# Performance work log

Measured on AMD Instinct MI355X. Metric: run time of the kernel, lower is better.

The kernel has to match this reference:

```python
import jax, jax.numpy as jnp
import numpy as np

N_SUPPORT = 4096
N_QUERY = 8192
H = W = 28
IN_DIM = H * W  # 784
EMBED_DIM = 512
N_CLASSES = 64


def setup_inputs() -> dict:
    key = jax.random.key(0)
    k1, k2, k3, k4 = jax.random.split(key, 4)
    support_set = jax.random.normal(k1, (N_SUPPORT, 1, H, W), dtype=jnp.float32)
    query_set = jax.random.normal(k2, (N_QUERY, 1, H, W), dtype=jnp.float32)
    # one-hot support labels (N, C)
    lbl = jax.random.randint(k3, (N_SUPPORT,), 0, N_CLASSES)
    support_labels = jax.nn.one_hot(lbl, N_CLASSES, dtype=jnp.float32)
    # encoder params: flatten + dense projection stand-in for embedding_net
    W_enc = jax.random.normal(k4, (IN_DIM, EMBED_DIM), dtype=jnp.float32) * (1.0 / np.sqrt(IN_DIM))
    b_enc = jnp.zeros((EMBED_DIM,), dtype=jnp.float32)
    return {
        "support_set": support_set,
        "query_set": query_set,
        "support_labels": support_labels,
        "W_enc": W_enc,
        "b_enc": b_enc,
    }


def _encode(x, W_enc, b_enc):
    # (B, 1, H, W) -> (B, D): flatten + linear projection
    B = x.shape[0]
    return x.reshape(B, -1) @ W_enc + b_enc


def _neg_cdist(q, s):
    # -euclidean distance, computed via the expansion ||q-s||^2 = |q|^2 + |s|^2 - 2 q.s
    q2 = jnp.sum(q * q, axis=-1, keepdims=True)          # (Q, 1)
    s2 = jnp.sum(s * s, axis=-1)[None, :]                # (1, N)
    qs = jnp.einsum("qd,nd->qn", q, s)                  # (Q, N)
    d2 = jnp.maximum(q2 + s2 - 2.0 * qs, 0.0)
    return -jnp.sqrt(d2)


def reference(support_set, query_set, support_labels, W_enc, b_enc):
    support_emb = _encode(support_set, W_enc, b_enc)     # (N, D)
    query_emb = _encode(query_set, W_enc, b_enc)         # (Q, D)
    distances = _neg_cdist(query_emb, support_emb)       # (Q, N)
    attention = jax.nn.softmax(distances, axis=1)        # (Q, N)
    predictions = attention @ support_labels             # (Q, C)
    return predictions
```

## Files before the change

### kernel.cpp

```cpp
#include <hip/hip_runtime.h>

#define N_SUP 4096
#define N_QRY 8192
#define IN_DIM 784
#define EMB 512
#define NCLS 64
#define M_TOT (N_SUP + N_QRY)
#define NCHUNK 25
#define XCH 13

typedef _Float16 f16;
typedef _Float16 f16x8 __attribute__((ext_vector_type(8)));
typedef float f32x4 __attribute__((ext_vector_type(4)));

#define GLDS16(gp, lp)                                                        \
    __builtin_amdgcn_global_load_lds(                                         \
        (const __attribute__((address_space(1))) void*)(gp),                  \
        (__attribute__((address_space(3))) void*)(lp), 16, 0, 0)

#define WAITB(N)                                                              \
    asm volatile("s_waitcnt vmcnt(" #N ")" ::: "memory");                     \
    __builtin_amdgcn_s_barrier();                                             \
    __builtin_amdgcn_sched_barrier(0);

static __device__ __forceinline__ f16x8 cvt8(const float* p) {
    float4 a = *(const float4*)p;
    float4 b = *(const float4*)(p + 4);
    f16x8 v;
    v[0] = (f16)a.x; v[1] = (f16)a.y; v[2] = (f16)a.z; v[3] = (f16)a.w;
    v[4] = (f16)b.x; v[5] = (f16)b.y; v[6] = (f16)b.z; v[7] = (f16)b.w;
    return v;
}

__global__ __launch_bounds__(256) void pre_enc(const float* __restrict__ W,
                                               const float* __restrict__ lab,
                                               f16* __restrict__ Wb,
                                               int* __restrict__ lbl) {
    if (blockIdx.x < 200) {
        int g = blockIdx.x * 256 + threadIdx.x;
        if (g >= NCHUNK * 32 * 64) return;
        int chunk = g >> 11;
        int rem = g & 2047;
        int nbg = rem >> 6, lane = rem & 63;
        int n = nbg * 16 + (lane & 15);
        int kbase = chunk * 32 + (lane >> 4) * 8;
        f16x8 v;
#pragma unroll
        for (int j = 0; j < 8; ++j) {
            int k = kbase + j;
            v[j] = (k < IN_DIM) ? (f16)W[(size_t)k * EMB + n] : (f16)0.f;
        }
        *(f16x8*)(Wb + (size_t)g * 8) = v;
    } else {
        const int w = threadIdx.x >> 6, lane = threadIdx.x & 63;
        const int s = (blockIdx.x - 200) * 4 + w;
        float v = lab[(size_t)s * NCLS + lane];
        int c = lane;
#pragma unroll
        for (int off = 1; off < 64; off <<= 1) {
            float v2 = __shfl_xor(v, off);
            int c2 = __shfl_xor(c, off);
            if (v2 > v || (v2 == v && c2 < c)) { v = v2; c = c2; }
        }
        if (lane == 0) lbl[s] = c;
    }
}

__global__ __launch_bounds__(256) void encode(
    const float* __restrict__ sup, const float* __restrict__ qry,
    const f16* __restrict__ Wb, const float* __restrict__ bias,
    f16* __restrict__ E, float* __restrict__ norms)
{
    __shared__ __align__(16) f16 Xs[32][72];
    const int tid = threadIdx.x;
    const int w = tid >> 6, lane = tid & 63;
    const int q = lane >> 4, c16 = lane & 15;
    const int mb = blockIdx.x >> 1;
    const int ch = blockIdx.x & 1;
    const int m0 = mb * 32;
    const int rbase = (w & 1) * 16;
    const int nbg0 = ch * 16 + (w >> 1) * 8;
    const int cbase = nbg0 * 16;

    f32x4 acc[8];
#pragma unroll
    for (int nb = 0; nb < 8; ++nb) acc[nb] = (f32x4){0.f, 0.f, 0.f, 0.f};

    const int sr = tid >> 3;
    const int sq = tid & 7;
    const float* xrow;
    {
        int gr = m0 + sr;
        xrow = (gr < N_SUP) ? sup + (size_t)gr * IN_DIM
                            : qry + (size_t)(gr - N_SUP) * IN_DIM;
    }

    f16x8 xg = cvt8(xrow + sq * 8);

    for (int c = 0; c < XCH; ++c) {
        __syncthreads();
        *(f16x8*)&Xs[sr][sq * 8] = xg;
        __syncthreads();
        if (c + 1 < XCH) {
            int k = (c + 1) * 64 + sq * 8;
            xg = (k + 8 <= IN_DIM) ? cvt8(xrow + k) : (f16x8){0,0,0,0,0,0,0,0};
        }
#pragma unroll
        for (int kc = 0; kc < 2; ++kc) {
            int c32 = c * 2 + kc;
            if (c32 >= NCHUNK) break;
            f16x8 a = *(const f16x8*)&Xs[rbase + c16][kc * 32 + q * 8];
            const f16* wb = Wb + ((size_t)(c32 * 32 + nbg0) * 64 + lane) * 8;
#pragma unroll
            for (int nb = 0; nb < 8; ++nb) {
                f16x8 b = *(const f16x8*)(wb + (size_t)nb * 512);
                acc[nb] = __builtin_amdgcn_mfma_f32_16x16x32_f16(a, b, acc[nb], 0, 0, 0);
            }
        }
    }

    float nrm[4] = {0.f, 0.f, 0.f, 0.f};
#pragma unroll
    for (int nb = 0; nb < 8; ++nb) {
        int col = cbase + nb * 16 + c16;
        float bv = bias[col];
#pragma unroll
        for (int r = 0; r < 4; ++r) {
            int row = m0 + rbase + q * 4 + r;
            float v = acc[nb][r] + bv;
            E[(size_t)row * EMB + col] = (f16)v;
            nrm[r] += v * v;
        }
    }
#pragma unroll
    for (int r = 0; r < 4; ++r) {
        float v = nrm[r];
        v += __shfl_xor(v, 1); v += __shfl_xor(v, 2);
        v += __shfl_xor(v, 4); v += __shfl_xor(v, 8);
        if (c16 == 0) atomicAdd(&norms[m0 + rbase + q * 4 + r], v);
    }
}

__global__ __launch_bounds__(256) void post_enc(
    const f16* __restrict__ E, const float* __restrict__ norms,
    const int* __restrict__ lbl, f16* __restrict__ Sb,
    f16* __restrict__ Lcs, float* __restrict__ manc)
{
    const int b = blockIdx.x;
    if (b < 1024) {
        int g = b * 256 + threadIdx.x;
        int s = g >> 6, lg = g & 63;
        f16x8 v = *(const f16x8*)(E + (size_t)s * EMB + lg * 8);
        *(f16x8*)(Sb + (size_t)s * EMB + ((lg ^ (s & 15)) * 8)) = v;
    } else if (b < 3072) {
        const int w = threadIdx.x >> 6, lane = threadIdx.x & 63;
        const int qrow = (b - 1024) * 4 + w;
        f16x8 qv = *(const f16x8*)(E + (size_t)(N_SUP + qrow) * EMB + lane * 8);
        f16x8 sv = *(const f16x8*)(E + lane * 8);
        float dot = 0.f;
#pragma unroll
        for (int j = 0; j < 8; ++j) dot += (float)qv[j] * (float)sv[j];
        dot += __shfl_xor(dot, 1);  dot += __shfl_xor(dot, 2);
        dot += __shfl_xor(dot, 4);  dot += __shfl_xor(dot, 8);
        dot += __shfl_xor(dot, 16); dot += __shfl_xor(dot, 32);
        if (lane == 0) {
            float d2 = fmaxf(norms[N_SUP + qrow] + norms[0] - 2.f * dot, 0.f);
            manc[qrow] = sqrtf(d2);
        }
    } else {
        int idx = (b - 3072) * 256 + threadIdx.x;
        int c = idx >> 12, s = idx & (N_SUP - 1);
        Lcs[idx] = (lbl[s] == c) ? (f16)1.f : (f16)0.f;
    }
}

__global__ __launch_bounds__(256, 2) void attn(
    const f16* __restrict__ E, const float* __restrict__ norms,
    const float* __restrict__ manc, const f16* __restrict__ Lcs,
    const f16* __restrict__ Sb, float* __restrict__ Num)
{
    __shared__ __align__(16) f16 Ss[4][16 * EMB];
    __shared__ __align__(16) f16 Pt[4][16][40];
    __shared__ float Sn[512];
    const int tid = threadIdx.x;
    const int w = tid >> 6, lane = tid & 63;
    const int q = lane >> 4, c16 = lane & 15;
    const int ss = blockIdx.x & 7;
    const int qt = blockIdx.x >> 3;

    Sn[tid]       = norms[ss * 512 + tid];
    Sn[256 + tid] = norms[ss * 512 + 256 + tid];

    f16x8 qf[16];
    const f16* qb = E + (size_t)(N_SUP + qt * 64 + w * 16 + c16) * EMB + q * 8;
#pragma unroll
    for (int ks = 0; ks < 16; ++ks) qf[ks] = *(const f16x8*)(qb + ks * 32);
    float q2[4], mrow[4];
#pragma unroll
    for (int r = 0; r < 4; ++r) {
        q2[r]   = norms[N_SUP + qt * 64 + w * 16 + q * 4 + r];
        mrow[r] = manc[qt * 64 + w * 16 + q * 4 + r];
    }

    f32x4 accPL[4];
#pragma unroll
    for (int nb = 0; nb < 4; ++nb) accPL[nb] = (f32x4){0.f, 0.f, 0.f, 0.f};

    const f16* sb_base = Sb + (size_t)(ss * 512) * EMB;
    const int wslot = w * 256;

    auto ISSUE = [&](int tt) {
        const f16* gsrc = sb_base + (size_t)tt * 16 * EMB;
#pragma unroll
        for (int i = 0; i < 4; ++i)
            GLDS16(gsrc + (size_t)(wslot + i * 64 + lane) * 8,
                   &Ss[tt & 3][(wslot + i * 64) * 8]);
    };
    auto BL = [&](int p, f16x8* bl) {
        const int ps0 = ss * 512 + p * 32;
#pragma unroll
        for (int nbc = 0; nbc < 4; ++nbc)
            bl[nbc] = *(const f16x8*)(Lcs + (size_t)(nbc * 16 + c16) * N_SUP + ps0 + q * 8);
    };
    auto QK = [&](int t) -> f32x4 {
        f32x4 a = (f32x4){0.f, 0.f, 0.f, 0.f};
        const f16* S = &Ss[t & 3][0];
#pragma unroll
        for (int kc = 0; kc < 4; ++kc)
#pragma unroll
            for (int ksl = 0; ksl < 4; ++ksl) {
                const int lg = kc * 16 + ksl * 4 + q;
                f16x8 b = *(const f16x8*)&S[c16 * EMB + ((lg ^ c16) * 8)];
                a = __builtin_amdgcn_mfma_f32_16x16x32_f16(qf[kc * 4 + ksl], b, a, 0, 0, 0);
            }
        return a;
    };
    auto EPI = [&](f32x4 acc, int t) {
        const float s2 = Sn[t * 16 + c16];
        const int pcol = (t & 1) * 16 + c16;
#pragma unroll
        for (int r = 0; r < 4; ++r) {
            float d2 = fmaxf(q2[r] + s2 - 2.f * acc[r], 0.f);
            float p = __expf(mrow[r] - __builtin_amdgcn_sqrtf(d2));
            Pt[w][q * 4 + r][pcol] = (f16)fminf(p, 60000.f);
        }
    };
    auto PV = [&](const f16x8* bl) {
        f16x8 af = *(const f16x8*)&Pt[w][c16][q * 8];
#pragma unroll
        for (int nbc = 0; nbc < 4; ++nbc)
            accPL[nbc] = __builtin_amdgcn_mfma_f32_16x16x32_f16(af, bl[nbc], accPL[nbc], 0, 0, 0);
    };

    ISSUE(0); ISSUE(1); ISSUE(2);
    asm volatile("s_waitcnt lgkmcnt(0)" ::: "memory");

    f16x8 bl[4];
    for (int tp = 0; tp < 14; ++tp) {
        const int t0 = tp * 2;
        WAITB(8);
        BL(tp, bl);
        ISSUE(t0 + 3);
        EPI(QK(t0), t0);
        WAITB(8);
        ISSUE(t0 + 4);
        EPI(QK(t0 + 1), t0 + 1);
        PV(bl);
    }
    WAITB(8); BL(14, bl); ISSUE(31); EPI(QK(28), 28);
    WAITB(8); EPI(QK(29), 29); PV(bl);
    WAITB(4); BL(15, bl); EPI(QK(30), 30);
    WAITB(0); EPI(QK(31), 31); PV(bl);

#pragma unroll
    for (int nbc = 0; nbc < 4; ++nbc)
#pragma unroll
        for (int r = 0; r < 4; ++r)
            atomicAdd(&Num[(size_t)(qt * 64 + w * 16 + q * 4 + r) * NCLS + nbc * 16 + c16],
                      accPL[nbc][r]);
}

__global__ __launch_bounds__(256) void finalize(const float* __restrict__ Num,
                                                float* __restrict__ out) {
    const int tid = threadIdx.x;
    const int w = tid >> 6, lane = tid & 63;
    const int qrow = blockIdx.x * 4 + w;
    float v = Num[(size_t)qrow * NCLS + lane];
    float s = v;
    s += __shfl_xor(s, 1);  s += __shfl_xor(s, 2);  s += __shfl_xor(s, 4);
    s += __shfl_xor(s, 8);  s += __shfl_xor(s, 16); s += __shfl_xor(s, 32);
    out[(size_t)qrow * NCLS + lane] = v / s;
}

extern "C" void kernel_launch(void* const* d_in, const int* in_sizes, int n_in,
                              void* d_out, int out_size, void* d_ws, size_t ws_size,
                              hipStream_t stream) {
    (void)in_sizes; (void)n_in; (void)out_size; (void)ws_size;
    const float* sup  = (const float*)d_in[0];
    const float* qry  = (const float*)d_in[1];
    const float* lab  = (const float*)d_in[2];
    const float* Wenc = (const float*)d_in[3];
    const float* benc = (const float*)d_in[4];
    float* out = (float*)d_out;

    char* ws = (char*)d_ws;
    size_t off = 0;
    f16* Wb = (f16*)(ws + off);        off += (size_t)NCHUNK * 32 * 64 * 8 * 2;
    f16* E  = (f16*)(ws + off);        off += (size_t)M_TOT * EMB * 2;
    f16* Sb = (f16*)(ws + off);        off += (size_t)N_SUP * EMB * 2;
    int* lbl = (int*)(ws + off);       off += (size_t)N_SUP * 4;
    f16* Lcs = (f16*)(ws + off);       off += (size_t)NCLS * N_SUP * 2;
    float* manc = (float*)(ws + off);  off += (size_t)N_QRY * 4;
    float* norms = (float*)(ws + off); off += (size_t)M_TOT * 4;
    float* Num = (float*)(ws + off);   off += (size_t)N_QRY * NCLS * 4;

    hipMemsetAsync(norms, 0, (size_t)M_TOT * 4 + (size_t)N_QRY * NCLS * 4, stream);

    pre_enc<<<1224, 256, 0, stream>>>(Wenc, lab, Wb, lbl);
    encode<<<M_TOT / 32 * 2, 256, 0, stream>>>(sup, qry, Wb, benc, E, norms);
    post_enc<<<4096, 256, 0, stream>>>(E, norms, lbl, Sb, Lcs, manc);
    attn<<<N_QRY / 64 * 8, 256, 0, stream>>>(E, norms, manc, Lcs, Sb, Num);
    finalize<<<N_QRY / 4, 256, 0, stream>>>(Num, out);
}
```

Baseline: 198.9 us.

## Fuse memset, anchor-distance and finalize into neighbouring kernels

Workspace zeroing (norms, Num, and a new per-tile counter) moves into extra blocks of pre_enc, replacing the hipMemsetAsync. The per-query anchor distance to support 0 is now computed inside attn from the already-loaded query fragments instead of in post_enc. The final row normalisation is done by the last of the eight attn blocks per query tile, using a threadfence and an atomic counter, which removes the finalize launch. Together these cut launches and intermediate global traffic, at the cost of extra redundant dot-product work per attn block and a serialized tail in the last block.

```diff
diff --git a/kernel.cpp b/kernel.cpp
--- a/kernel.cpp
+++ b/kernel.cpp
@@ -35,7 +35,8 @@
 __global__ __launch_bounds__(256) void pre_enc(const float* __restrict__ W,
                                                const float* __restrict__ lab,
                                                f16* __restrict__ Wb,
-                                               int* __restrict__ lbl) {
+                                               int* __restrict__ lbl,
+                                               float4* __restrict__ zbase) {
     if (blockIdx.x < 200) {
         int g = blockIdx.x * 256 + threadIdx.x;
         if (g >= NCHUNK * 32 * 64) return;
@@ -51,7 +52,7 @@
             v[j] = (k < IN_DIM) ? (f16)W[(size_t)k * EMB + n] : (f16)0.f;
         }
         *(f16x8*)(Wb + (size_t)g * 8) = v;
-    } else {
+    } else if (blockIdx.x < 1224) {
         const int w = threadIdx.x >> 6, lane = threadIdx.x & 63;
         const int s = (blockIdx.x - 200) * 4 + w;
         float v = lab[(size_t)s * NCLS + lane];
@@ -63,6 +64,9 @@
             if (v2 > v || (v2 == v && c2 < c)) { v = v2; c = c2; }
         }
         if (lane == 0) lbl[s] = c;
+    } else {
+        int idx = (blockIdx.x - 1224) * 256 + threadIdx.x;
+        zbase[idx] = (float4){0.f, 0.f, 0.f, 0.f};
     }
 }
 
@@ -142,9 +146,8 @@
 }
 
 __global__ __launch_bounds__(256) void post_enc(
-    const f16* __restrict__ E, const float* __restrict__ norms,
-    const int* __restrict__ lbl, f16* __restrict__ Sb,
-    f16* __restrict__ Lcs, float* __restrict__ manc)
+    const f16* __restrict__ E, const int* __restrict__ lbl,
+    f16* __restrict__ Sb, f16* __restrict__ Lcs)
 {
     const int b = blockIdx.x;
     if (b < 1024) {
@@ -152,23 +155,8 @@
         int s = g >> 6, lg = g & 63;
         f16x8 v = *(const f16x8*)(E + (size_t)s * EMB + lg * 8);
         *(f16x8*)(Sb + (size_t)s * EMB + ((lg ^ (s & 15)) * 8)) = v;
-    } else if (b < 3072) {
-        const int w = threadIdx.x >> 6, lane = threadIdx.x & 63;
-        const int qrow = (b - 1024) * 4 + w;
-        f16x8 qv = *(const f16x8*)(E + (size_t)(N_SUP + qrow) * EMB + lane * 8);
-        f16x8 sv = *(const f16x8*)(E + lane * 8);
-        float dot = 0.f;
-#pragma unroll
-        for (int j = 0; j < 8; ++j) dot += (float)qv[j] * (float)sv[j];
-        dot += __shfl_xor(dot, 1);  dot += __shfl_xor(dot, 2);
-        dot += __shfl_xor(dot, 4);  dot += __shfl_xor(dot, 8);
-        dot += __shfl_xor(dot, 16); dot += __shfl_xor(dot, 32);
-        if (lane == 0) {
-            float d2 = fmaxf(norms[N_SUP + qrow] + norms[0] - 2.f * dot, 0.f);
-            manc[qrow] = sqrtf(d2);
-        }
     } else {
-        int idx = (b - 3072) * 256 + threadIdx.x;
+        int idx = (b - 1024) * 256 + threadIdx.x;
         int c = idx >> 12, s = idx & (N_SUP - 1);
         Lcs[idx] = (lbl[s] == c) ? (f16)1.f : (f16)0.f;
     }
@@ -176,12 +164,14 @@
 
 __global__ __launch_bounds__(256, 2) void attn(
     const f16* __restrict__ E, const float* __restrict__ norms,
-    const float* __restrict__ manc, const f16* __restrict__ Lcs,
-    const f16* __restrict__ Sb, float* __restrict__ Num)
+    const f16* __restrict__ Lcs, const f16* __restrict__ Sb,
+    float* __restrict__ Num, int* __restrict__ cnt, float* __restrict__ out)
 {
     __shared__ __align__(16) f16 Ss[4][16 * EMB];
     __shared__ __align__(16) f16 Pt[4][16][40];
     __shared__ float Sn[512];
+    __shared__ float Manc[4][16];
+    __shared__ int lastf;
     const int tid = threadIdx.x;
     const int w = tid >> 6, lane = tid & 63;
     const int q = lane >> 4, c16 = lane & 15;
@@ -195,11 +185,27 @@
     const f16* qb = E + (size_t)(N_SUP + qt * 64 + w * 16 + c16) * EMB + q * 8;
 #pragma unroll
     for (int ks = 0; ks < 16; ++ks) qf[ks] = *(const f16x8*)(qb + ks * 32);
+
+    {
+        float n0 = norms[0];
+        float dp = 0.f;
+        const f16* s0p = E + q * 8;
+#pragma unroll
+        for (int ks = 0; ks < 16; ++ks) {
+            f16x8 sv = *(const f16x8*)(s0p + ks * 32);
+#pragma unroll
+            for (int j = 0; j < 8; ++j) dp += (float)qf[ks][j] * (float)sv[j];
+        }
+        dp += __shfl_xor(dp, 16);
+        dp += __shfl_xor(dp, 32);
+        float qn = norms[N_SUP + qt * 64 + w * 16 + c16];
+        Manc[w][c16] = __builtin_amdgcn_sqrtf(fmaxf(qn + n0 - 2.f * dp, 0.f));
+    }
     float q2[4], mrow[4];
 #pragma unroll
     for (int r = 0; r < 4; ++r) {
         q2[r]   = norms[N_SUP + qt * 64 + w * 16 + q * 4 + r];
-        mrow[r] = manc[qt * 64 + w * 16 + q * 4 + r];
+        mrow[r] = Manc[w][q * 4 + r];
     }
 
     f32x4 accPL[4];
@@ -278,18 +284,23 @@
         for (int r = 0; r < 4; ++r)
             atomicAdd(&Num[(size_t)(qt * 64 + w * 16 + q * 4 + r) * NCLS + nbc * 16 + c16],
                       accPL[nbc][r]);
-}
-
-__global__ __launch_bounds__(256) void finalize(const float* __restrict__ Num,
-                                                float* __restrict__ out) {
-    const int tid = threadIdx.x;
-    const int w = tid >> 6, lane = tid & 63;
-    const int qrow = blockIdx.x * 4 + w;
-    float v = Num[(size_t)qrow * NCLS + lane];
-    float s = v;
-    s += __shfl_xor(s, 1);  s += __shfl_xor(s, 2);  s += __shfl_xor(s, 4);
-    s += __shfl_xor(s, 8);  s += __shfl_xor(s, 16); s += __shfl_xor(s, 32);
-    out[(size_t)qrow * NCLS + lane] = v / s;
+
+    __threadfence();
+    if (tid == 0) lastf = (atomicAdd(cnt + qt, 1) == 7) ? 1 : 0;
+    __syncthreads();
+    if (lastf) {
+        const float* Nq = Num + (size_t)(qt * 64) * NCLS;
+        float* oq = out + (size_t)(qt * 64) * NCLS;
+#pragma unroll
+        for (int i = 0; i < 16; ++i) {
+            int row = w * 16 + i;
+            float v = Nq[row * NCLS + lane];
+            float s = v;
+            s += __shfl_xor(s, 1);  s += __shfl_xor(s, 2);  s += __shfl_xor(s, 4);
+            s += __shfl_xor(s, 8);  s += __shfl_xor(s, 16); s += __shfl_xor(s, 32);
+            oq[row * NCLS + lane] = v / s;
+        }
+    }
 }
 
 extern "C" void kernel_launch(void* const* d_in, const int* in_sizes, int n_in,
@@ -310,15 +321,12 @@
     f16* Sb = (f16*)(ws + off);        off += (size_t)N_SUP * EMB * 2;
     int* lbl = (int*)(ws + off);       off += (size_t)N_SUP * 4;
     f16* Lcs = (f16*)(ws + off);       off += (size_t)NCLS * N_SUP * 2;
-    float* manc = (float*)(ws + off);  off += (size_t)N_QRY * 4;
     float* norms = (float*)(ws + off); off += (size_t)M_TOT * 4;
     float* Num = (float*)(ws + off);   off += (size_t)N_QRY * NCLS * 4;
-
-    hipMemsetAsync(norms, 0, (size_t)M_TOT * 4 + (size_t)N_QRY * NCLS * 4, stream);
-
-    pre_enc<<<1224, 256, 0, stream>>>(Wenc, lab, Wb, lbl);
+    int* cnt = (int*)(ws + off);       off += 32768;
+
+    pre_enc<<<1756, 256, 0, stream>>>(Wenc, lab, Wb, lbl, (float4*)norms);
     encode<<<M_TOT / 32 * 2, 256, 0, stream>>>(sup, qry, Wb, benc, E, norms);
-    post_enc<<<4096, 256, 0, stream>>>(E, norms, lbl, Sb, Lcs, manc);
-    attn<<<N_QRY / 64 * 8, 256, 0, stream>>>(E, norms, manc, Lcs, Sb, Num);
-    finalize<<<N_QRY / 4, 256, 0, stream>>>(Num, out);
-}
+    post_enc<<<2048, 256, 0, stream>>>(E, lbl, Sb, Lcs);
+    attn<<<N_QRY / 64 * 8, 256, 0, stream>>>(E, norms, Lcs, Sb, Num, cnt, out);
+}
```

After: 266.0 us. 33.8% more time.
